# Performance work log

Measured on AMD Instinct MI355X. Metric: run time of the kernel, lower is better.

The kernel has to match this reference:

```python
import jax, jax.numpy as jnp
import numpy as np

B, S, D = 4, 2048, 1024
H, DK, DV = 16, 64, 64


def setup_inputs() -> dict:
    key = jax.random.key(0)
    ks = jax.random.split(key, 9)
    std = 1.0 / np.sqrt(D)
    inp = {
        "x": jax.random.normal(ks[0], (B, S, D), jnp.float32),
        "c": jax.random.normal(ks[1], (B, S, D), jnp.float32),
        "Wq_x": jax.random.normal(ks[2], (D, H * DK), jnp.float32) * std,
        "Wk_x": jax.random.normal(ks[3], (D, H * DK), jnp.float32) * std,
        "Wv_x": jax.random.normal(ks[4], (D, H * DV), jnp.float32) * std,
        "Wq_c": jax.random.normal(ks[5], (D, H * DK), jnp.float32) * std,
        "Wk_c": jax.random.normal(ks[6], (D, H * DK), jnp.float32) * std,
        "Wv_c": jax.random.normal(ks[7], (D, H * DV), jnp.float32) * std,
        "W_proj": jax.random.normal(ks[8], (2 * H * DV, D), jnp.float32) * (1.0 / np.sqrt(2 * H * DV)),
        "b_proj": jnp.zeros((D,), jnp.float32),
    }
    return inp


def _heads(t, hd):
    # [B,S,H*hd] -> [B,H,S,hd]
    b, s, _ = t.shape
    return t.reshape(b, s, H, hd).transpose(0, 2, 1, 3)


def reference(x, c, Wq_x, Wk_x, Wv_x, Wq_c, Wk_c, Wv_c, W_proj, b_proj):
    q = jnp.concatenate([_heads(x @ Wq_x, DK), _heads(c @ Wq_c, DK)], axis=-1)  # [B,H,S,2DK]
    k = jnp.concatenate([_heads(x @ Wk_x, DK), _heads(c @ Wk_c, DK)], axis=-1)
    v = jnp.concatenate([_heads(x @ Wv_x, DV), _heads(c @ Wv_c, DV)], axis=-1)  # [B,H,S,2DV]
    # NOTE: original scales by sqrt(k_dim), not sqrt(2*k_dim) (faithful)
    scores = jnp.einsum("bhqd,bhkd->bhqk", q, k) / np.float32(np.sqrt(DK))
    attn = jax.nn.softmax(scores, axis=-1)
    out = jnp.einsum("bhqk,bhkd->bhqd", attn, v)  # [B,H,S,2DV]
    out = out.transpose(0, 2, 1, 3).reshape(x.shape[0], x.shape[1], -1)  # [B,S,H*2DV]
    return out @ W_proj + b_proj
```

## Files before the change

kernel.cpp:

```cpp
#include <hip/hip_runtime.h>
#include <hip/hip_bf16.h>
#include <stdint.h>

#define BB 4
#define SS 2048
#define DD 1024
#define HH 16
#define DHH 128

typedef __bf16 bf16x8 __attribute__((ext_vector_type(8)));
typedef __bf16 bf16x4 __attribute__((ext_vector_type(4)));
typedef float  f32x4  __attribute__((ext_vector_type(4)));

#define SL2E 0.180336880111186f

#if __has_builtin(__builtin_amdgcn_exp2f)
#define EXP2(x) __builtin_amdgcn_exp2f(x)
#else
#define EXP2(x) exp2f(x)
#endif

#define GLOAD_LDS16(gp, lp) \
  __builtin_amdgcn_global_load_lds((const __attribute__((address_space(1))) unsigned int*)(gp), \
                                   (__attribute__((address_space(3))) unsigned int*)(lp), 16, 0, 0)

#define SBAR() do { asm volatile("" ::: "memory"); \
                    __builtin_amdgcn_s_barrier();  \
                    asm volatile("" ::: "memory"); } while (0)

#define MFMA_BF16(a, b, c) __builtin_amdgcn_mfma_f32_16x16x32_bf16((a), (b), (c), 0, 0, 0)

__global__ void cast2_kernel(const float* __restrict__ x, const float* __restrict__ c,
                             __bf16* __restrict__ out, int n) {
    int i = (blockIdx.x * blockDim.x + threadIdx.x) * 4;
    const float* src = (i < n) ? (x + i) : (c + (i - n));
    f32x4 v = *(const f32x4*)src;
    bf16x4 o;
    o[0] = (__bf16)v[0]; o[1] = (__bf16)v[1]; o[2] = (__bf16)v[2]; o[3] = (__bf16)v[3];
    *(bf16x4*)(out + i) = o;
}

__global__ void transpose_cast_kernel(const float* __restrict__ in, __bf16* __restrict__ out,
                                      int K, int N) {
    __shared__ float tile[32][33];
    int n0 = blockIdx.x * 32, k0 = blockIdx.y * 32;
    int tx = threadIdx.x, ty = threadIdx.y;
    #pragma unroll
    for (int i = 0; i < 32; i += 8)
        tile[ty + i][tx] = in[(size_t)(k0 + ty + i) * N + n0 + tx];
    __syncthreads();
    #pragma unroll
    for (int i = 0; i < 32; i += 8)
        out[(size_t)(n0 + ty + i) * K + k0 + tx] = (__bf16)tile[tx][ty + i];
}

__global__ void transpose6_kernel(const float* s0, const float* s1, const float* s2,
                                  const float* s3, const float* s4, const float* s5,
                                  __bf16* __restrict__ dst) {
    const float* srcs[6] = {s0, s1, s2, s3, s4, s5};
    const float* __restrict__ in = srcs[blockIdx.z];
    __bf16* __restrict__ out = dst + (size_t)blockIdx.z * 1024 * 1024;
    __shared__ float tile[32][33];
    int n0 = blockIdx.x * 32, k0 = blockIdx.y * 32;
    int tx = threadIdx.x, ty = threadIdx.y;
    #pragma unroll
    for (int i = 0; i < 32; i += 8)
        tile[ty + i][tx] = in[(size_t)(k0 + ty + i) * 1024 + n0 + tx];
    __syncthreads();
    #pragma unroll
    for (int i = 0; i < 32; i += 8)
        out[(size_t)(n0 + ty + i) * 1024 + k0 + tx] = (__bf16)tile[tx][ty + i];
}

template <int EPI>
__global__ __launch_bounds__(512, 2)
void gemm256_kernel(const __bf16* __restrict__ A0, const __bf16* __restrict__ A1,
                    const __bf16* __restrict__ B0, const __bf16* __restrict__ B1,
                    int K, void* __restrict__ outp, const float* __restrict__ bias) {
    const int z = blockIdx.z;
    const __bf16* __restrict__ A  = z ? A1 : A0;
    const __bf16* __restrict__ Bt = z ? B1 : B0;
    const int qkv_off = z * 64;

    __shared__ __align__(16) char smem[131072];

    const int tid = threadIdx.x;
    const int wave = tid >> 6, lane = tid & 63;
    const int l15 = lane & 15, quad = lane >> 4;
    const int wr = wave >> 2, wc = wave & 3;

    const int gx = gridDim.x;
    const int nwg = gx * gridDim.y;
    const int hwl = blockIdx.y * gx + blockIdx.x;
    const int lg  = (hwl & 7) * (nwg >> 3) + (hwl >> 3);
    const int m0 = (lg % gx) * 256, n0 = (lg / gx) * 256;

    const int rA = tid >> 2;
    const int cs = (tid & 3) ^ ((tid >> 4) & 3);
    const __bf16* aS0 = A  + (size_t)(m0 + rA) * K + cs * 8;
    const __bf16* aS1 = aS0 + (size_t)128 * K;
    const __bf16* bS0 = Bt + (size_t)(n0 + rA) * K + cs * 8;
    const __bf16* bS1 = bS0 + (size_t)128 * K;
    const int ldsA = wave * 1024;
    const int ldsB = 16384 + wave * 1024;

    const int swz = ((quad ^ (l15 >> 2)) & 3) * 16;
    const int ra = (wr * 128 + l15) * 64 + swz;
    const int rb = 16384 + (wc * 64 + l15) * 64 + swz;

    f32x4 acc[8][4] = {};
    bf16x8 afc[2][4], bfc[2][4], afB[4];
    const int NT = K >> 5;

    #define STAGE_A(tt) do { const int bo_ = ((tt) & 3) * 32768; \
        GLOAD_LDS16(aS0 + (size_t)(tt) * 32, smem + bo_ + ldsA); \
        GLOAD_LDS16(aS1 + (size_t)(tt) * 32, smem + bo_ + ldsA + 8192); } while (0)
    #define STAGE_B(tt) do { const int bo_ = ((tt) & 3) * 32768; \
        GLOAD_LDS16(bS0 + (size_t)(tt) * 32, smem + bo_ + ldsB); \
        GLOAD_LDS16(bS1 + (size_t)(tt) * 32, smem + bo_ + ldsB + 8192); } while (0)

    STAGE_A(0); STAGE_B(0);
    STAGE_A(1); STAGE_B(1);
    STAGE_A(2); STAGE_B(2);
    asm volatile("s_waitcnt vmcnt(8)" ::: "memory");
    SBAR();
    #pragma unroll
    for (int i = 0; i < 4; ++i) afc[0][i] = *(const bf16x8*)(smem + ra + i * 1024);
    #pragma unroll
    for (int i = 0; i < 4; ++i) bfc[0][i] = *(const bf16x8*)(smem + rb + i * 1024);

    for (int tp = 0; tp < NT / 2; ++tp) {
        #pragma unroll
        for (int u = 0; u < 2; ++u) {
            const int t = 2 * tp + u;
            const int co = (t & 3) * 32768;
            const int cn = ((t + 1) & 3) * 32768;
            #pragma unroll
            for (int i = 0; i < 4; ++i)
                afB[i] = *(const bf16x8*)(smem + co + ra + (4 + i) * 1024);
            if (t + 3 < NT) STAGE_A(t + 3);
            SBAR();
            __builtin_amdgcn_s_setprio(1);
            #pragma unroll
            for (int mi = 0; mi < 4; ++mi)
                #pragma unroll
                for (int ni = 0; ni < 4; ++ni)
                    acc[mi][ni] = MFMA_BF16(afc[u][mi], bfc[u][ni], acc[mi][ni]);
            __builtin_amdgcn_s_setprio(0);
            if (t + 3 < NT) STAGE_B(t + 3);
            if (t < NT - 3)       asm volatile("s_waitcnt vmcnt(8)" ::: "memory");
            else if (t == NT - 3) asm volatile("s_waitcnt vmcnt(4)" ::: "memory");
            else if (t == NT - 2) asm volatile("s_waitcnt vmcnt(0)" ::: "memory");
            SBAR();
            #pragma unroll
            for (int i = 0; i < 4; ++i)
                afc[u ^ 1][i] = *(const bf16x8*)(smem + cn + ra + i * 1024);
            #pragma unroll
            for (int i = 0; i < 4; ++i)
                bfc[u ^ 1][i] = *(const bf16x8*)(smem + cn + rb + i * 1024);
            __builtin_amdgcn_s_setprio(1);
            #pragma unroll
            for (int mi = 0; mi < 4; ++mi)
                #pragma unroll
                for (int ni = 0; ni < 4; ++ni)
                    acc[4 + mi][ni] = MFMA_BF16(afB[mi], bfc[u][ni], acc[4 + mi][ni]);
            __builtin_amdgcn_s_setprio(0);
        }
    }
    #undef STAGE_A
    #undef STAGE_B

    const size_t nQKV = (size_t)BB * HH * SS * DHH;
    #pragma unroll
    for (int mi = 0; mi < 8; ++mi) {
        #pragma unroll
        for (int ni = 0; ni < 4; ++ni) {
            #pragma unroll
            for (int rr = 0; rr < 4; ++rr) {
                int m = m0 + wr * 128 + mi * 16 + quad * 4 + rr;
                int n = n0 + wc * 64 + ni * 16 + l15;
                if (EPI == 2) {
                    int h = m >> 6, dl = m & 63;
                    int b = n >> 11, s = n & (SS - 1);
                    __bf16* vt = (__bf16*)outp;
                    vt[(((size_t)b * HH + h) * DHH + dl + qkv_off) * SS + s] = (__bf16)acc[mi][ni][rr];
                } else {
                    int b = m >> 11, s = m & (SS - 1);
                    int n1 = n & 1023;
                    int h = n1 >> 6, d = (n1 & 63) + qkv_off;
                    if (n < 1024) {
                        __bf16* q = (__bf16*)outp;
                        q[(((size_t)b * HH + h) * SS + s) * DHH + d] = (__bf16)(acc[mi][ni][rr] * SL2E);
                    } else {
                        int dsw = (((d >> 3) ^ (s & 15)) << 3) | (d & 7);
                        __bf16* kq = (__bf16*)outp + nQKV;
                        kq[(((size_t)b * HH + h) * SS + s) * DHH + dsw] = (__bf16)acc[mi][ni][rr];
                    }
                }
            }
        }
    }
}

__global__ __launch_bounds__(512, 2)
void gemm_proj_kernel(const __bf16* __restrict__ A, const __bf16* __restrict__ Bt,
                      int K, float* __restrict__ outp, const float* __restrict__ bias) {
    __shared__ __align__(16) char smem[98304];

    const int tid = threadIdx.x;
    const int wave = tid >> 6, lane = tid & 63;
    const int l15 = lane & 15, quad = lane >> 4;
    const int wr = wave >> 1, wc = wave & 1;

    const int gx = gridDim.x;
    const int nwg = gx * gridDim.y;
    const int hwl = blockIdx.y * gx + blockIdx.x;
    const int lg  = (hwl & 7) * (nwg >> 3) + (hwl >> 3);
    const int m0 = (lg % gx) * 256, n0 = (lg / gx) * 128;

    const int rA = tid >> 2;
    const int cs = (tid & 3) ^ ((tid >> 4) & 3);
    const __bf16* aS0 = A  + (size_t)(m0 + rA) * K + cs * 8;
    const __bf16* aS1 = aS0 + (size_t)128 * K;
    const __bf16* bS0 = Bt + (size_t)(n0 + rA) * K + cs * 8;
    const int ldsA = wave * 1024;
    const int ldsB = 16384 + wave * 1024;

    const int swz = ((quad ^ (l15 >> 2)) & 3) * 16;
    const int ra = (wr * 64 + l15) * 64 + swz;
    const int rb = 16384 + (wc * 64 + l15) * 64 + swz;

    f32x4 acc[4][4] = {};
    bf16x8 afc[2][4], bfc[2][4];
    const int NT = K >> 5;

    #define STAGE_P(tt) do { const int bo_ = ((tt) & 3) * 24576; \
        GLOAD_LDS16(aS0 + (size_t)(tt) * 32, smem + bo_ + ldsA); \
        GLOAD_LDS16(aS1 + (size_t)(tt) * 32, smem + bo_ + ldsA + 8192); \
        GLOAD_LDS16(bS0 + (size_t)(tt) * 32, smem + bo_ + ldsB); } while (0)

    STAGE_P(0); STAGE_P(1); STAGE_P(2);
    asm volatile("s_waitcnt vmcnt(6)" ::: "memory");
    SBAR();
    #pragma unroll
    for (int i = 0; i < 4; ++i) afc[0][i] = *(const bf16x8*)(smem + ra + i * 1024);
    #pragma unroll
    for (int i = 0; i < 4; ++i) bfc[0][i] = *(const bf16x8*)(smem + rb + i * 1024);

    for (int tp = 0; tp < NT / 2; ++tp) {
        #pragma unroll
        for (int u = 0; u < 2; ++u) {
            const int t = 2 * tp + u;
            const int cn = ((t + 1) & 3) * 24576;
            if (t + 3 < NT) STAGE_P(t + 3);
            if (t < NT - 3)       asm volatile("s_waitcnt vmcnt(6)" ::: "memory");
            else if (t == NT - 3) asm volatile("s_waitcnt vmcnt(3)" ::: "memory");
            else if (t == NT - 2) asm volatile("s_waitcnt vmcnt(0)" ::: "memory");
            SBAR();
            #pragma unroll
            for (int i = 0; i < 4; ++i)
                afc[u ^ 1][i] = *(const bf16x8*)(smem + cn + ra + i * 1024);
            #pragma unroll
            for (int i = 0; i < 4; ++i)
                bfc[u ^ 1][i] = *(const bf16x8*)(smem + cn + rb + i * 1024);
            __builtin_amdgcn_s_setprio(1);
            #pragma unroll
            for (int mi = 0; mi < 4; ++mi)
                #pragma unroll
                for (int ni = 0; ni < 4; ++ni)
                    acc[mi][ni] = MFMA_BF16(afc[u][mi], bfc[u][ni], acc[mi][ni]);
            __builtin_amdgcn_s_setprio(0);
        }
    }
    #undef STAGE_P

    #pragma unroll
    for (int mi = 0; mi < 4; ++mi)
        #pragma unroll
        for (int ni = 0; ni < 4; ++ni)
            #pragma unroll
            for (int rr = 0; rr < 4; ++rr) {
                int m = m0 + wr * 64 + mi * 16 + quad * 4 + rr;
                int n = n0 + wc * 64 + ni * 16 + l15;
                outp[(size_t)m * 1024 + n] = acc[mi][ni][rr] + bias[n];
            }
}

#define LDS_BUFSZ 32768
#define LDS_VT    16384
#define LDS_PS    65536
__global__ __launch_bounds__(256, 2)
void attn_kernel(const __bf16* __restrict__ Q, const __bf16* __restrict__ Kg,
                 const __bf16* __restrict__ Vg, __bf16* __restrict__ O) {
    __shared__ __align__(16) char smem[73728];

    const int t = threadIdx.x;
    const int wave = t >> 6, lane = t & 63;
    const int l15 = lane & 15, quad = lane >> 4;

    const int lin = blockIdx.x;
    const int mt = (lin >> 3) & 15;
    const int bh = ((lin >> 7) << 3) + (lin & 7);

    const int b = bh >> 4, h = bh & 15;
    const size_t base  = (size_t)bh * SS * DHH;
    const size_t vbase = (size_t)bh * DHH * SS;

    int kaddr[4];
    #pragma unroll
    for (int kst = 0; kst < 4; ++kst)
        kaddr[kst] = l15 * 256 + (((4 * kst + quad) ^ l15) & 15) * 16;
    int vaddr[2];
    #pragma unroll
    for (int hf = 0; hf < 2; ++hf)
        vaddr[hf] = LDS_VT + l15 * 128 + (((4 * hf + quad) ^ (l15 & 7)) & 7) * 16;
    int pw[2];
    #pragma unroll
    for (int nl = 0; nl < 2; ++nl)
        pw[nl] = LDS_PS + (wave * 32 + quad * 4) * 64 +
                 (((2 * nl + (l15 >> 3)) ^ quad) & 3) * 16 + (l15 & 7) * 2;
    const int par = LDS_PS + (wave * 32 + l15) * 64 + ((quad ^ (l15 >> 2)) & 3) * 16;

    const __bf16* kstage = Kg + base + (size_t)wave * 2048 + lane * 8;
    const __bf16* vstage = Vg + vbase + (size_t)(wave * 32 + (lane >> 3)) * SS
                           + ((lane & 7) ^ ((lane >> 3) & 7)) * 8;

    #define STAGE_KV(kt_, bo_) do { \
        _Pragma("unroll") \
        for (int i_ = 0; i_ < 4; ++i_) \
            GLOAD_LDS16(kstage + (size_t)(kt_) * 8192 + i_ * 512, \
                        smem + (bo_) + wave * 4096 + i_ * 1024); \
        _Pragma("unroll") \
        for (int i_ = 0; i_ < 4; ++i_) \
            GLOAD_LDS16(vstage + (kt_) * 64 + (size_t)i_ * 8 * SS, \
                        smem + (bo_) + LDS_VT + wave * 4096 + i_ * 1024); \
    } while (0)

    bf16x8 qf[2][4];
    #pragma unroll
    for (int ms = 0; ms < 2; ++ms) {
        int row = mt * 128 + wave * 32 + ms * 16 + l15;
        #pragma unroll
        for (int kst = 0; kst < 4; ++kst)
            qf[ms][kst] = *(const bf16x8*)(Q + base + (size_t)row * DHH + kst * 32 + quad * 8);
    }

    f32x4 oacc[2][8] = {};
    float li_[2][4] = {};

    STAGE_KV(0, 0);
    __syncthreads();

    for (int kt = 0; kt < SS / 64; ++kt) {
        const int co = (kt & 1) * LDS_BUFSZ;
        if (kt + 1 < SS / 64) STAGE_KV(kt + 1, co ^ LDS_BUFSZ);

        #pragma unroll
        for (int hf = 0; hf < 2; ++hf) {
            f32x4 sx[2][2] = {};
            __builtin_amdgcn_s_setprio(1);
            #pragma unroll
            for (int kst = 0; kst < 4; ++kst) {
                bf16x8 kf0 = *(const bf16x8*)(smem + co + kaddr[kst] + 8192 * hf);
                bf16x8 kf1 = *(const bf16x8*)(smem + co + kaddr[kst] + 8192 * hf + 4096);
                sx[0][0] = MFMA_BF16(qf[0][kst], kf0, sx[0][0]);
                sx[1][0] = MFMA_BF16(qf[1][kst], kf0, sx[1][0]);
                sx[0][1] = MFMA_BF16(qf[0][kst], kf1, sx[0][1]);
                sx[1][1] = MFMA_BF16(qf[1][kst], kf1, sx[1][1]);
            }
            __builtin_amdgcn_s_setprio(0);
            #pragma unroll
            for (int ms = 0; ms < 2; ++ms)
                #pragma unroll
                for (int nl = 0; nl < 2; ++nl)
                    #pragma unroll
                    for (int rr = 0; rr < 4; ++rr) {
                        float p = EXP2(sx[ms][nl][rr]);
                        li_[ms][rr] += p;
                        sx[ms][nl][rr] = p;
                    }

            #pragma unroll
            for (int ms = 0; ms < 2; ++ms)
                #pragma unroll
                for (int nl = 0; nl < 2; ++nl)
                    #pragma unroll
                    for (int rr = 0; rr < 4; ++rr)
                        *(__bf16*)(smem + pw[nl] + 1024 * ms + 64 * rr)
                            = (__bf16)sx[ms][nl][rr];

            bf16x8 pa0 = *(const bf16x8*)(smem + par);
            bf16x8 pa1 = *(const bf16x8*)(smem + par + 1024);
            __builtin_amdgcn_s_setprio(1);
            #pragma unroll
            for (int ds = 0; ds < 8; ++ds) {
                bf16x8 vf = *(const bf16x8*)(smem + co + vaddr[hf] + 2048 * ds);
                oacc[0][ds] = MFMA_BF16(pa0, vf, oacc[0][ds]);
                oacc[1][ds] = MFMA_BF16(pa1, vf, oacc[1][ds]);
            }
            __builtin_amdgcn_s_setprio(0);
        }
        __syncthreads();
    }
    #undef STAGE_KV

    #pragma unroll
    for (int ms = 0; ms < 2; ++ms)
        #pragma unroll
        for (int rr = 0; rr < 4; ++rr) {
            float v = li_[ms][rr];
            v += __shfl_xor(v, 1);
            v += __shfl_xor(v, 2);
            v += __shfl_xor(v, 4);
            v += __shfl_xor(v, 8);
            li_[ms][rr] = 1.f / v;
        }

    #pragma unroll
    for (int ms = 0; ms < 2; ++ms)
        #pragma unroll
        for (int rr = 0; rr < 4; ++rr) {
            int s = mt * 128 + wave * 32 + ms * 16 + quad * 4 + rr;
            size_t ob = ((size_t)b * SS + s) * (HH * DHH) + (size_t)h * DHH;
            #pragma unroll
            for (int ds = 0; ds < 8; ++ds)
                O[ob + ds * 16 + l15] = (__bf16)(oacc[ms][ds][rr] * li_[ms][rr]);
        }
}

extern "C" void kernel_launch(void* const* d_in, const int* in_sizes, int n_in,
                              void* d_out, int out_size, void* d_ws, size_t ws_size,
                              hipStream_t stream) {
    const float* x      = (const float*)d_in[0];
    const float* c      = (const float*)d_in[1];
    const float* Wq_x   = (const float*)d_in[2];
    const float* Wk_x   = (const float*)d_in[3];
    const float* Wv_x   = (const float*)d_in[4];
    const float* Wq_c   = (const float*)d_in[5];
    const float* Wk_c   = (const float*)d_in[6];
    const float* Wv_c   = (const float*)d_in[7];
    const float* W_proj = (const float*)d_in[8];
    const float* b_proj = (const float*)d_in[9];

    const size_t nXC  = (size_t)BB * SS * DD;
    const size_t nW   = (size_t)DD * DD;
    const size_t nWP  = (size_t)(2 * HH * 64) * DD;
    const size_t nQKV = (size_t)BB * HH * SS * DHH;

    __bf16* ws  = (__bf16*)d_ws;
    __bf16* xb  = ws;
    __bf16* cb  = xb + nXC;
    __bf16* wt0 = cb + nXC;
    __bf16* wt2 = wt0 + 2 * nW;
    __bf16* wt3 = wt0 + 3 * nW;
    __bf16* wt5 = wt0 + 5 * nW;
    __bf16* wtp = wt0 + 6 * nW;
    __bf16* Qb  = wtp + nWP;
    __bf16* Kb  = Qb + nQKV;
    __bf16* Vb  = Kb + nQKV;
    __bf16* Ob  = xb;

    cast2_kernel<<<(int)(2 * nXC / 1024), 256, 0, stream>>>(x, c, xb, (int)nXC);

    transpose6_kernel<<<dim3(32, 32, 6), dim3(32, 8), 0, stream>>>(
        Wq_x, Wk_x, Wv_x, Wq_c, Wk_c, Wv_c, wt0);
    transpose_cast_kernel<<<dim3(32, 64), dim3(32, 8), 0, stream>>>(W_proj, wtp, 2048, 1024);

    gemm256_kernel<4><<<dim3(32, 8, 2), 512, 0, stream>>>(xb, cb, wt0, wt3, 1024, Qb, nullptr);
    gemm256_kernel<2><<<dim3(4, 32, 2), 512, 0, stream>>>(wt2, wt5, xb, cb, 1024, Vb, nullptr);

    attn_kernel<<<dim3(1024), 256, 0, stream>>>(Qb, Kb, Vb, Ob);

    gemm_proj_kernel<<<dim3(32, 8), 512, 0, stream>>>(Ob, wtp, 2048, (float*)d_out, b_proj);
}
```

Baseline: 447.5 us.

## Double attention query tile to 256 rows per block for K/V reuse

Each attention block now processes 256 query rows (64 per wave) instead of 128, halving the grid and the number of times each K/V tile is loaded into LDS. The S computation is reorganized to loop over key subtiles with four query subtiles each, writing P straight to LDS. This trades higher register use (larger accumulators and Q fragments) and fewer blocks in flight for less global/LDS K/V traffic.

```diff
diff --git a/kernel.cpp b/kernel.cpp
--- a/kernel.cpp
+++ b/kernel.cpp
@@ -292,15 +292,15 @@
 __global__ __launch_bounds__(256, 2)
 void attn_kernel(const __bf16* __restrict__ Q, const __bf16* __restrict__ Kg,
                  const __bf16* __restrict__ Vg, __bf16* __restrict__ O) {
-    __shared__ __align__(16) char smem[73728];
+    __shared__ __align__(16) char smem[81920];
 
     const int t = threadIdx.x;
     const int wave = t >> 6, lane = t & 63;
     const int l15 = lane & 15, quad = lane >> 4;
 
     const int lin = blockIdx.x;
-    const int mt = (lin >> 3) & 15;
-    const int bh = ((lin >> 7) << 3) + (lin & 7);
+    const int mt = (lin >> 3) & 7;
+    const int bh = ((lin >> 6) << 3) + (lin & 7);
 
     const int b = bh >> 4, h = bh & 15;
     const size_t base  = (size_t)bh * SS * DHH;
@@ -317,9 +317,9 @@
     int pw[2];
     #pragma unroll
     for (int nl = 0; nl < 2; ++nl)
-        pw[nl] = LDS_PS + (wave * 32 + quad * 4) * 64 +
+        pw[nl] = LDS_PS + (wave * 64 + quad * 4) * 64 +
                  (((2 * nl + (l15 >> 3)) ^ quad) & 3) * 16 + (l15 & 7) * 2;
-    const int par = LDS_PS + (wave * 32 + l15) * 64 + ((quad ^ (l15 >> 2)) & 3) * 16;
+    const int par = LDS_PS + (wave * 64 + l15) * 64 + ((quad ^ (l15 >> 2)) & 3) * 16;
 
     const __bf16* kstage = Kg + base + (size_t)wave * 2048 + lane * 8;
     const __bf16* vstage = Vg + vbase + (size_t)(wave * 32 + (lane >> 3)) * SS
@@ -336,17 +336,17 @@
                         smem + (bo_) + LDS_VT + wave * 4096 + i_ * 1024); \
     } while (0)
 
-    bf16x8 qf[2][4];
-    #pragma unroll
-    for (int ms = 0; ms < 2; ++ms) {
-        int row = mt * 128 + wave * 32 + ms * 16 + l15;
+    bf16x8 qf[4][4];
+    #pragma unroll
+    for (int ms = 0; ms < 4; ++ms) {
+        int row = mt * 256 + wave * 64 + ms * 16 + l15;
         #pragma unroll
         for (int kst = 0; kst < 4; ++kst)
             qf[ms][kst] = *(const bf16x8*)(Q + base + (size_t)row * DHH + kst * 32 + quad * 8);
     }
 
-    f32x4 oacc[2][8] = {};
-    float li_[2][4] = {};
+    f32x4 oacc[4][8] = {};
+    float li_[4][4] = {};
 
     STAGE_KV(0, 0);
     __syncthreads();
@@ -357,46 +357,41 @@
 
         #pragma unroll
         for (int hf = 0; hf < 2; ++hf) {
-            f32x4 sx[2][2] = {};
-            __builtin_amdgcn_s_setprio(1);
-            #pragma unroll
-            for (int kst = 0; kst < 4; ++kst) {
-                bf16x8 kf0 = *(const bf16x8*)(smem + co + kaddr[kst] + 8192 * hf);
-                bf16x8 kf1 = *(const bf16x8*)(smem + co + kaddr[kst] + 8192 * hf + 4096);
-                sx[0][0] = MFMA_BF16(qf[0][kst], kf0, sx[0][0]);
-                sx[1][0] = MFMA_BF16(qf[1][kst], kf0, sx[1][0]);
-                sx[0][1] = MFMA_BF16(qf[0][kst], kf1, sx[0][1]);
-                sx[1][1] = MFMA_BF16(qf[1][kst], kf1, sx[1][1]);
-            }
-            __builtin_amdgcn_s_setprio(0);
-            #pragma unroll
-            for (int ms = 0; ms < 2; ++ms)
+            #pragma unroll
+            for (int nl = 0; nl < 2; ++nl) {
+                f32x4 sxn[4] = {};
+                __builtin_amdgcn_s_setprio(1);
                 #pragma unroll
-                for (int nl = 0; nl < 2; ++nl)
+                for (int kst = 0; kst < 4; ++kst) {
+                    bf16x8 kf = *(const bf16x8*)(smem + co + kaddr[kst] + 8192 * hf + 4096 * nl);
+                    sxn[0] = MFMA_BF16(qf[0][kst], kf, sxn[0]);
+                    sxn[1] = MFMA_BF16(qf[1][kst], kf, sxn[1]);
+                    sxn[2] = MFMA_BF16(qf[2][kst], kf, sxn[2]);
+                    sxn[3] = MFMA_BF16(qf[3][kst], kf, sxn[3]);
+                }
+                __builtin_amdgcn_s_setprio(0);
+                #pragma unroll
+                for (int ms = 0; ms < 4; ++ms)
                     #pragma unroll
                     for (int rr = 0; rr < 4; ++rr) {
-                        float p = EXP2(sx[ms][nl][rr]);
+                        float p = EXP2(sxn[ms][rr]);
                         li_[ms][rr] += p;
-                        sx[ms][nl][rr] = p;
+                        *(__bf16*)(smem + pw[nl] + 1024 * ms + 64 * rr) = (__bf16)p;
                     }
-
-            #pragma unroll
-            for (int ms = 0; ms < 2; ++ms)
-                #pragma unroll
-                for (int nl = 0; nl < 2; ++nl)
-                    #pragma unroll
-                    for (int rr = 0; rr < 4; ++rr)
-                        *(__bf16*)(smem + pw[nl] + 1024 * ms + 64 * rr)
-                            = (__bf16)sx[ms][nl][rr];
-
-            bf16x8 pa0 = *(const bf16x8*)(smem + par);
-            bf16x8 pa1 = *(const bf16x8*)(smem + par + 1024);
+            }
+
+            bf16x8 pa[4];
+            #pragma unroll
+            for (int ms = 0; ms < 4; ++ms)
+                pa[ms] = *(const bf16x8*)(smem + par + 1024 * ms);
             __builtin_amdgcn_s_setprio(1);
             #pragma unroll
             for (int ds = 0; ds < 8; ++ds) {
                 bf16x8 vf = *(const bf16x8*)(smem + co + vaddr[hf] + 2048 * ds);
-                oacc[0][ds] = MFMA_BF16(pa0, vf, oacc[0][ds]);
-                oacc[1][ds] = MFMA_BF16(pa1, vf, oacc[1][ds]);
+                oacc[0][ds] = MFMA_BF16(pa[0], vf, oacc[0][ds]);
+                oacc[1][ds] = MFMA_BF16(pa[1], vf, oacc[1][ds]);
+                oacc[2][ds] = MFMA_BF16(pa[2], vf, oacc[2][ds]);
+                oacc[3][ds] = MFMA_BF16(pa[3], vf, oacc[3][ds]);
             }
             __builtin_amdgcn_s_setprio(0);
         }
@@ -405,7 +400,7 @@
     #undef STAGE_KV
 
     #pragma unroll
-    for (int ms = 0; ms < 2; ++ms)
+    for (int ms = 0; ms < 4; ++ms)
         #pragma unroll
         for (int rr = 0; rr < 4; ++rr) {
             float v = li_[ms][rr];
@@ -417,10 +412,10 @@
         }
 
     #pragma unroll
-    for (int ms = 0; ms < 2; ++ms)
+    for (int ms = 0; ms < 4; ++ms)
         #pragma unroll
         for (int rr = 0; rr < 4; ++rr) {
-            int s = mt * 128 + wave * 32 + ms * 16 + quad * 4 + rr;
+            int s = mt * 256 + wave * 64 + ms * 16 + quad * 4 + rr;
             size_t ob = ((size_t)b * SS + s) * (HH * DHH) + (size_t)h * DHH;
             #pragma unroll
             for (int ds = 0; ds < 8; ++ds)
@@ -469,7 +464,7 @@
     gemm256_kernel<4><<<dim3(32, 8, 2), 512, 0, stream>>>(xb, cb, wt0, wt3, 1024, Qb, nullptr);
     gemm256_kernel<2><<<dim3(4, 32, 2), 512, 0, stream>>>(wt2, wt5, xb, cb, 1024, Vb, nullptr);
 
-    attn_kernel<<<dim3(1024), 256, 0, stream>>>(Qb, Kb, Vb, Ob);
+    attn_kernel<<<dim3(512), 256, 0, stream>>>(Qb, Kb, Vb, Ob);
 
     gemm_proj_kernel<<<dim3(32, 8), 512, 0, stream>>>(Ob, wtp, 2048, (float*)d_out, b_proj);
 }
```

New measurement: 447.3 us. No clear change (-0.1%).
